# Performance work log

Measured on AMD Instinct MI355X. Metric: run time of the kernel, lower is better.

Reference implementation:

```python
import jax, jax.numpy as jnp
import numpy as np

H = 8
DH = 64  # attention_head_size
HID = 512
NEG = -90000000000.0

def _lin(x, w, b):
    return x @ w + b

def _tfs(x):  # [N, HID] -> [H, N, DH]
    n = x.shape[0]
    return x.reshape(n, H, DH).transpose(1, 0, 2)

def _cross(q, ck, v, cv, mask, dw, db):
    # q: [H,N,DH], ck/cv: [H,M,DH], v: [H,N,DH], mask: [N,M]
    s = jnp.einsum('hnd,hmd->hnm', q, ck)
    s = s * mask[None, :, :] / jnp.sqrt(jnp.asarray(DH, s.dtype))
    s = jnp.where(s == 0.0, NEG, s)  # faithful zero->-inf hack
    p = jax.nn.softmax(s, axis=-1)
    ctx = v + jnp.einsum('hnm,hmd->hnd', p, cv)  # residual add of raw value
    n = ctx.shape[1]
    ctx = ctx.transpose(1, 0, 2).reshape(n, H * DH)
    return _lin(ctx, dw, db)

def setup_inputs() -> dict:
    key = jax.random.key(0)
    ks = jax.random.split(key, 24)
    N1, N2, D1 = 4096, 4096, 300
    d = {}
    d['h_head'] = jax.random.normal(ks[0], (N1, D1), jnp.float32)
    d['h_tail'] = jax.random.normal(ks[1], (N2, HID), jnp.float32)
    d['batch_head'] = jnp.sort(jax.random.randint(ks[2], (N1,), 0, 64))
    d['batch_tail'] = jnp.sort(jax.random.randint(ks[3], (N2,), 0, 64))
    def w(k, i, o):
        return jax.random.normal(k, (i, o), jnp.float32) / np.sqrt(i)
    d['map_w'] = w(ks[4], D1, HID); d['map_b'] = jnp.zeros((HID,), jnp.float32)
    names = ['q1', 'k1', 'v1', 'q2', 'k2', 'v2', 'd1', 'd2']
    for i, nm in enumerate(names):
        d[nm + '_w'] = w(ks[5 + i], HID, HID)
        d[nm + '_b'] = jnp.zeros((HID,), jnp.float32)
    return d

def reference(h_head, h_tail, batch_head, batch_tail,
              map_w, map_b,
              q1_w, q1_b, k1_w, k1_b, v1_w, v1_b,
              q2_w, q2_b, k2_w, k2_b, v2_w, v2_b,
              d1_w, d1_b, d2_w, d2_b):
    hh = _lin(h_head, map_w, map_b)  # n_dim1 != n_dim2 -> map
    q_h = _tfs(_lin(hh, q1_w, q1_b))
    k_h = _tfs(_lin(hh, k1_w, k1_b))
    v_h = _tfs(_lin(hh, v1_w, v1_b))
    q_t = _tfs(_lin(h_tail, q2_w, q2_b))
    k_t = _tfs(_lin(h_tail, k2_w, k2_b))
    v_t = _tfs(_lin(h_tail, v2_w, v2_b))
    mask = (batch_head[:, None] == batch_tail[None, :]).astype(jnp.float32)
    out_head = _cross(q_h, k_t, v_h, v_t, mask, d1_w, d1_b)
    out_tail = _cross(q_t, k_h, v_t, v_h, mask.T, d2_w, d2_b)
    return (out_head, out_tail)
```

## Files before the change

kernel.cpp:

```cpp
#include <hip/hip_runtime.h>
#include <hip/hip_bf16.h>
#include <math.h>


typedef __bf16 bf16x8 __attribute__((ext_vector_type(8)));
typedef float  f32x4  __attribute__((ext_vector_type(4)));

#define HID 512
#define NTOK 4096

#define AS1(p) ((const __attribute__((address_space(1))) void*)(p))
#define AS3(p) ((__attribute__((address_space(3))) void*)(p))

struct PrepArgs {
    const float* h_head; const float* h_tail;
    const int* bh; const int* bt;
    const float* map_w; const float* map_b;
    const float* qkvw[3]; const float* qkvb[3];
    const float* tsrc[8]; __bf16* tdst[8];
    __bf16* hh_bf; __bf16* ht_bf; __bf16* mapw_bf;
    float* fb;
    int* ranges;
};

__global__ __launch_bounds__(256) void fused_prep(PrepArgs pa) {
    const int q = blockIdx.x, z = blockIdx.z, tid = threadIdx.x;
    __shared__ __bf16 T[64][72];

    if (z == 0) {
        if (q == 0 && tid < 128) {
            int b = tid & 63;
            const int* arr = (tid < 64) ? pa.bh : pa.bt;
            int base = (tid < 64) ? 0 : 128;
            int lo = 0, hi = NTOK;
            while (lo < hi) { int mid = (lo + hi) >> 1; if (arr[mid] < b) lo = mid + 1; else hi = mid; }
            int start = lo;
            lo = 0; hi = NTOK;
            while (lo < hi) { int mid = (lo + hi) >> 1; if (arr[mid] <= b) lo = mid + 1; else hi = mid; }
            pa.ranges[base + b] = start;
            pa.ranges[base + 64 + b] = lo;
        }
        for (int idx = tid; idx < 8 * 40; idx += 256) {
            int r   = q * 8 + idx / 40;
            int col = (idx % 40) * 8;
            bf16x8 v;
            if (col + 8 <= 300) {
                float4 f0 = *(const float4*)&pa.h_head[(size_t)r * 300 + col];
                float4 f1 = *(const float4*)&pa.h_head[(size_t)r * 300 + col + 4];
                v[0]=(__bf16)f0.x; v[1]=(__bf16)f0.y; v[2]=(__bf16)f0.z; v[3]=(__bf16)f0.w;
                v[4]=(__bf16)f1.x; v[5]=(__bf16)f1.y; v[6]=(__bf16)f1.z; v[7]=(__bf16)f1.w;
            } else if (col < 300) {
                float4 f0 = *(const float4*)&pa.h_head[(size_t)r * 300 + col];
                v[0]=(__bf16)f0.x; v[1]=(__bf16)f0.y; v[2]=(__bf16)f0.z; v[3]=(__bf16)f0.w;
                v[4]=(__bf16)0.f; v[5]=(__bf16)0.f; v[6]=(__bf16)0.f; v[7]=(__bf16)0.f;
            } else {
                #pragma unroll
                for (int j = 0; j < 8; ++j) v[j] = (__bf16)0.f;
            }
            *(bf16x8*)&pa.hh_bf[(size_t)r * 320 + col] = v;
        }
    } else if (z == 1) {
        for (int idx = tid; idx < 8 * 64; idx += 256) {
            int r   = q * 8 + (idx >> 6);
            int col = (idx & 63) * 8;
            float4 f0 = *(const float4*)&pa.h_tail[(size_t)r * 512 + col];
            float4 f1 = *(const float4*)&pa.h_tail[(size_t)r * 512 + col + 4];
            bf16x8 v;
            v[0]=(__bf16)f0.x; v[1]=(__bf16)f0.y; v[2]=(__bf16)f0.z; v[3]=(__bf16)f0.w;
            v[4]=(__bf16)f1.x; v[5]=(__bf16)f1.y; v[6]=(__bf16)f1.z; v[7]=(__bf16)f1.w;
            *(bf16x8*)&pa.ht_bf[(size_t)r * 512 + col] = v;
        }
    } else if (z == 2) {
        if (q < 96) {
            int r   = q * 4 + (tid >> 6);
            int col = (tid & 63) * 8;
            bf16x8 v;
            if (r < 300) {
                float4 f0 = *(const float4*)&pa.map_w[(size_t)r * 512 + col];
                float4 f1 = *(const float4*)&pa.map_w[(size_t)r * 512 + col + 4];
                v[0]=(__bf16)f0.x; v[1]=(__bf16)f0.y; v[2]=(__bf16)f0.z; v[3]=(__bf16)f0.w;
                v[4]=(__bf16)f1.x; v[5]=(__bf16)f1.y; v[6]=(__bf16)f1.z; v[7]=(__bf16)f1.w;
            } else {
                #pragma unroll
                for (int j = 0; j < 8; ++j) v[j] = (__bf16)0.f;
            }
            *(bf16x8*)&pa.mapw_bf[(size_t)r * 512 + col] = v;
        } else if (q < 102) {
            int b2 = q - 96;
            int w  = b2 >> 1;
            int n  = ((b2 & 1) << 8) + tid;
            const float* W = pa.qkvw[w];
            float s = pa.qkvb[w][n];
            for (int j = 0; j < 512; ++j)
                s += pa.map_b[j] * W[(size_t)j * 512 + n];
            pa.fb[w * 512 + n] = s;
        }
    } else {
        if (q >= 64) return;
        const int jz = z - 3;
        const float* src = pa.tsrc[jz];
        __bf16* dst = pa.tdst[jz];
        const int tk = (q >> 3) * 64;
        const int tn = (q & 7) * 64;
        const int r0 = tid >> 4;
        const int c0 = (tid & 15) * 4;
        #pragma unroll
        for (int i = 0; i < 4; ++i) {
            float4 v = *(const float4*)&src[(size_t)(tk + r0 + i * 16) * 512 + tn + c0];
            T[r0 + i * 16][c0 + 0] = (__bf16)v.x;
            T[r0 + i * 16][c0 + 1] = (__bf16)v.y;
            T[r0 + i * 16][c0 + 2] = (__bf16)v.z;
            T[r0 + i * 16][c0 + 3] = (__bf16)v.w;
        }
        __syncthreads();
        const int n  = tid >> 2;
        const int kk = (tid & 3) * 16;
        bf16x8 o0, o1;
        #pragma unroll
        for (int j = 0; j < 8; ++j) { o0[j] = T[kk + j][n]; o1[j] = T[kk + 8 + j][n]; }
        __bf16* dp = dst + (size_t)(tn + n) * 512 + tk + kk;
        *(bf16x8*)dp       = o0;
        *(bf16x8*)(dp + 8) = o1;
    }
}

struct GemmJobs {
    const __bf16* A[6];
    const __bf16* W[6];
    const float*  bias[6];
    void*         C[6];
    int           Kp[6];
    int           ldC[6];
    int           Ncol[6];
};

template <typename TC>
__global__ __launch_bounds__(256) void gemm128(GemmJobs jobs) {
    __shared__ __align__(16) __bf16 As[2][4096];
    __shared__ __align__(16) __bf16 Bs[2][4096];

    const int z = blockIdx.z;
    const __bf16* A    = jobs.A[z];
    const __bf16* W    = jobs.W[z];
    const float*  bias = jobs.bias[z];
    TC*           C    = (TC*)jobs.C[z];
    const int     Kp   = jobs.Kp[z];

    const int tid  = threadIdx.x;
    const int wave = tid >> 6;
    const int lane = tid & 63;
    const int quad = lane >> 4;
    const int l16  = lane & 15;
    const int wy   = wave >> 1;
    const int wx   = wave & 1;
    const int rowBase = blockIdx.y * 128;
    const int colBase = blockIdx.x * 128;

    const int s_row = tid >> 2;
    const int s_kc  = ((tid & 3) ^ ((s_row >> 1) & 3)) * 8;

    const __bf16* gA = A + (size_t)(rowBase + s_row) * Kp + s_kc;
    const __bf16* gB = W + (size_t)(colBase + s_row) * Kp + s_kc;
    const int waveOff = wave * 512;

    f32x4 acc[4][4] = {};
    const int nk = Kp >> 5;

    __builtin_amdgcn_global_load_lds(AS1(gA),                   AS3(&As[0][waveOff]),        16, 0, 0);
    __builtin_amdgcn_global_load_lds(AS1(gA + (size_t)64 * Kp), AS3(&As[0][2048 + waveOff]), 16, 0, 0);
    __builtin_amdgcn_global_load_lds(AS1(gB),                   AS3(&Bs[0][waveOff]),        16, 0, 0);
    __builtin_amdgcn_global_load_lds(AS1(gB + (size_t)64 * Kp), AS3(&Bs[0][2048 + waveOff]), 16, 0, 0);

    for (int i = 0; i < nk; ++i) {
        const int cur = i & 1;
        __syncthreads();

        if (i + 1 < nk) {
            const int kt = (i + 1) * 32;
            const int nx = cur ^ 1;
            __builtin_amdgcn_global_load_lds(AS1(gA + kt),                   AS3(&As[nx][waveOff]),        16, 0, 0);
            __builtin_amdgcn_global_load_lds(AS1(gA + kt + (size_t)64 * Kp), AS3(&As[nx][2048 + waveOff]), 16, 0, 0);
            __builtin_amdgcn_global_load_lds(AS1(gB + kt),                   AS3(&Bs[nx][waveOff]),        16, 0, 0);
            __builtin_amdgcn_global_load_lds(AS1(gB + kt + (size_t)64 * Kp), AS3(&Bs[nx][2048 + waveOff]), 16, 0, 0);
        }

        bf16x8 ar[4], br[4];
        #pragma unroll
        for (int ii = 0; ii < 4; ++ii) {
            const int ra = wy * 64 + ii * 16 + l16;
            ar[ii] = *(const bf16x8*)&As[cur][ra * 32 + ((quad ^ ((ra >> 1) & 3)) << 3)];
        }
        #pragma unroll
        for (int jj = 0; jj < 4; ++jj) {
            const int rb = wx * 64 + jj * 16 + l16;
            br[jj] = *(const bf16x8*)&Bs[cur][rb * 32 + ((quad ^ ((rb >> 1) & 3)) << 3)];
        }
        #pragma unroll
        for (int ii = 0; ii < 4; ++ii)
            #pragma unroll
            for (int jj = 0; jj < 4; ++jj)
                acc[ii][jj] = __builtin_amdgcn_mfma_f32_16x16x32_bf16(ar[ii], br[jj], acc[ii][jj], 0, 0, 0);
    }

    const int ldC  = jobs.ldC[z];
    const int Ncol = jobs.Ncol[z];
    #pragma unroll
    for (int jj = 0; jj < 4; ++jj) {
        int col = colBase + wx * 64 + jj * 16 + l16;
        if (col < Ncol) {
            float bv = bias ? bias[col] : 0.f;
            #pragma unroll
            for (int ii = 0; ii < 4; ++ii) {
                #pragma unroll
                for (int r = 0; r < 4; ++r) {
                    int row = rowBase + wy * 64 + ii * 16 + quad * 4 + r;
                    C[(size_t)row * ldC + col] = (TC)(acc[ii][jj][r] + bv);
                }
            }
        }
    }
}

__global__ __launch_bounds__(256) void attn_mfma(
    const __bf16* __restrict__ Q0, const __bf16* __restrict__ K0,
    const __bf16* __restrict__ Vr0, const __bf16* __restrict__ Vc0,
    const __bf16* __restrict__ Q1, const __bf16* __restrict__ K1,
    const __bf16* __restrict__ Vr1, const __bf16* __restrict__ Vc1,
    const int* __restrict__ ranges,
    __bf16* __restrict__ O0, __bf16* __restrict__ O1,
    int Nq, int Nk)
{
    __shared__ __align__(16) __bf16 Qs[64][72];
    __shared__ __align__(16) __bf16 Ks[64][72];
    __shared__ __align__(16) __bf16 Vt[64][72];
    __shared__ __align__(16) __bf16 Ps[64][72];

    const int z = blockIdx.z;
    const __bf16* Q    = z ? Q1 : Q0;
    const __bf16* Kg   = z ? K1 : K0;
    const __bf16* Vres = z ? Vr1 : Vr0;
    const __bf16* Vctx = z ? Vc1 : Vc0;
    __bf16* Out        = z ? O1 : O0;
    const int* qstart  = z ? ranges + 128 : ranges;
    const int* qend    = z ? ranges + 192 : ranges + 64;
    const int* kstart  = z ? ranges       : ranges + 128;
    const int* kend    = z ? ranges + 64  : ranges + 192;

    const int h = blockIdx.x, b = blockIdx.y;
    const int qs = qstart[b], qe = qend[b];
    const int ts = kstart[b], te = kend[b];
    const int nq = qe - qs, nk = te - ts;
    if (nq <= 0) return;

    const int tid  = threadIdx.x;
    const int wave = tid >> 6;
    const int lane = tid & 63;
    const int quad = lane >> 4;
    const int l16  = lane & 15;
    const int srow = tid >> 2;
    const int scol = (tid & 3) * 16;

    if (nk <= 0) {
        float* meanv = (float*)Qs;
        if (tid < 64) {
            float s = 0.f;
            for (int m = 0; m < Nk; ++m)
                s += (float)Vctx[(size_t)m * HID + h * 64 + tid];
            meanv[tid] = s / (float)Nk;
        }
        __syncthreads();
        int d = tid & 63;
        for (int r = qs + (tid >> 6); r < qe; r += 4) {
            size_t off = (size_t)r * HID + h * 64 + d;
            Out[off] = (__bf16)((float)Vres[off] + meanv[d]);
        }
        return;
    }

    for (int qc = 0; qc < nq; qc += 64) {
        __syncthreads();
        {
            int qg = min(qs + qc + srow, Nq - 1);
            const __bf16* src = Q + (size_t)qg * HID + h * 64 + scol;
            *(bf16x8*)&Qs[srow][scol]     = *(const bf16x8*)src;
            *(bf16x8*)&Qs[srow][scol + 8] = *(const bf16x8*)(src + 8);
        }
        __syncthreads();
        bf16x8 aq0 = *(const bf16x8*)&Qs[wave * 16 + l16][quad * 8];
        bf16x8 aq1 = *(const bf16x8*)&Qs[wave * 16 + l16][32 + quad * 8];

        f32x4 O[4] = {};
        float Mx[4], L[4];
        #pragma unroll
        for (int r = 0; r < 4; ++r) { Mx[r] = -__builtin_inff(); L[r] = 0.f; }

// ... 75 lines not shown
            #pragma unroll
            for (int c = 0; c < 4; ++c)
                #pragma unroll
                for (int r = 0; r < 4; ++r)
                    Ps[wave * 16 + quad * 4 + r][c * 16 + l16] = (__bf16)S[c][r];
            __syncthreads();

            bf16x8 ap0 = *(const bf16x8*)&Ps[wave * 16 + l16][quad * 8];
            bf16x8 ap1 = *(const bf16x8*)&Ps[wave * 16 + l16][32 + quad * 8];
            #pragma unroll
            for (int c = 0; c < 4; ++c) {
                bf16x8 bv0 = *(const bf16x8*)&Vt[c * 16 + l16][quad * 8];
                bf16x8 bv1 = *(const bf16x8*)&Vt[c * 16 + l16][32 + quad * 8];
                O[c] = __builtin_amdgcn_mfma_f32_16x16x32_bf16(ap0, bv0, O[c], 0, 0, 0);
                O[c] = __builtin_amdgcn_mfma_f32_16x16x32_bf16(ap1, bv1, O[c], 0, 0, 0);
            }
        }

        #pragma unroll
        for (int c = 0; c < 4; ++c) {
            int d = h * 64 + c * 16 + l16;
            #pragma unroll
            for (int r = 0; r < 4; ++r) {
                int qrow = qs + qc + wave * 16 + quad * 4 + r;
                if (qrow < qe) {
                    size_t off = (size_t)qrow * HID + d;
                    Out[off] = (__bf16)((float)Vres[off] + O[c][r] / L[r]);
                }
            }
        }
    }
}

extern "C" void kernel_launch(void* const* d_in, const int* in_sizes, int n_in,
                              void* d_out, int out_size, void* d_ws, size_t ws_size,
                              hipStream_t stream) {
    (void)in_sizes; (void)n_in; (void)out_size; (void)ws_size;

    const float* h_head = (const float*)d_in[0];
    const float* h_tail = (const float*)d_in[1];
    const int* batch_head = (const int*)d_in[2];
    const int* batch_tail = (const int*)d_in[3];
    const float* map_w = (const float*)d_in[4];
    const float* map_b = (const float*)d_in[5];
    const float* q1_w = (const float*)d_in[6];
    const float* q1_b = (const float*)d_in[7];
    const float* k1_w = (const float*)d_in[8];
    const float* k1_b = (const float*)d_in[9];
    const float* v1_w = (const float*)d_in[10];
    const float* v1_b = (const float*)d_in[11];
    const float* q2_w = (const float*)d_in[12];
    const float* q2_b = (const float*)d_in[13];
    const float* k2_w = (const float*)d_in[14];
    const float* k2_b = (const float*)d_in[15];
    const float* v2_w = (const float*)d_in[16];
    const float* v2_b = (const float*)d_in[17];
    const float* d1_w = (const float*)d_in[18];
    const float* d1_b = (const float*)d_in[19];
    const float* d2_w = (const float*)d_in[20];
    const float* d2_b = (const float*)d_in[21];

    float* out = (float*)d_out;

    const size_t SZ = (size_t)NTOK * HID;
    char* ws = (char*)d_ws;
    int* ranges   = (int*)ws;
    __bf16* hh_bf = (__bf16*)(ws + 1024);
    __bf16* ht_bf = hh_bf + (size_t)NTOK * 320;
    __bf16* mapw_bf = ht_bf + SZ;
    __bf16* q1T  = mapw_bf + 384 * 512;
    __bf16* k1T  = q1T + 512 * 512;
    __bf16* v1T  = k1T + 512 * 512;
    __bf16* q2T  = v1T + 512 * 512;
    __bf16* k2T  = q2T + 512 * 512;
    __bf16* v2T  = k2T + 512 * 512;
    __bf16* d1T  = v2T + 512 * 512;
    __bf16* d2T  = d1T + 512 * 512;
    __bf16* FqT  = d2T + 512 * 512;
    __bf16* FkT  = FqT + 512 * 320;
    __bf16* FvT  = FkT + 512 * 320;
    __bf16* qh   = FvT + 512 * 320;
    __bf16* kh   = qh  + SZ;
    __bf16* vh   = kh  + SZ;
    __bf16* qt   = vh  + SZ;
    __bf16* kt   = qt  + SZ;
    __bf16* vt   = kt  + SZ;
    __bf16* ctxh = vt  + SZ;
    __bf16* ctxt = ctxh + SZ;
    float*  fb   = (float*)(ctxt + SZ);

    PrepArgs pa;
    pa.h_head = h_head; pa.h_tail = h_tail;
    pa.bh = batch_head; pa.bt = batch_tail;
    pa.map_w = map_w; pa.map_b = map_b;
    pa.qkvw[0] = q1_w; pa.qkvw[1] = k1_w; pa.qkvw[2] = v1_w;
    pa.qkvb[0] = q1_b; pa.qkvb[1] = k1_b; pa.qkvb[2] = v1_b;
    const float* wsrc[8] = {q1_w, k1_w, v1_w, q2_w, k2_w, v2_w, d1_w, d2_w};
    __bf16* wdst[8] = {q1T, k1T, v1T, q2T, k2T, v2T, d1T, d2T};
    for (int i = 0; i < 8; ++i) { pa.tsrc[i] = wsrc[i]; pa.tdst[i] = wdst[i]; }
    pa.hh_bf = hh_bf; pa.ht_bf = ht_bf; pa.mapw_bf = mapw_bf;
    pa.fb = fb; pa.ranges = ranges;
    fused_prep<<<dim3(512, 1, 11), dim3(256), 0, stream>>>(pa);

    {
        GemmJobs j;
        const __bf16* a3[3] = {q1T, k1T, v1T};
        __bf16* c3[3] = {FqT, FkT, FvT};
        for (int i = 0; i < 6; ++i) {
            int s = i < 3 ? i : 0;
            j.A[i] = a3[s]; j.W[i] = mapw_bf; j.bias[i] = nullptr;
            j.C[i] = c3[s]; j.Kp[i] = 512; j.ldC[i] = 320; j.Ncol[i] = 320;
        }
        gemm128<__bf16><<<dim3(3, 4, 3), dim3(256), 0, stream>>>(j);
    }

    {
        GemmJobs j;
        j.A[0] = hh_bf; j.W[0] = FqT; j.bias[0] = fb;        j.C[0] = qh; j.Kp[0] = 320;
        j.A[1] = hh_bf; j.W[1] = FkT; j.bias[1] = fb + 512;  j.C[1] = kh; j.Kp[1] = 320;
        j.A[2] = hh_bf; j.W[2] = FvT; j.bias[2] = fb + 1024; j.C[2] = vh; j.Kp[2] = 320;
        j.A[3] = ht_bf; j.W[3] = q2T; j.bias[3] = q2_b;      j.C[3] = qt; j.Kp[3] = 512;
        j.A[4] = ht_bf; j.W[4] = k2T; j.bias[4] = k2_b;      j.C[4] = kt; j.Kp[4] = 512;
        j.A[5] = ht_bf; j.W[5] = v2T; j.bias[5] = v2_b;      j.C[5] = vt; j.Kp[5] = 512;
        for (int i = 0; i < 6; ++i) { j.ldC[i] = HID; j.Ncol[i] = HID; }
        gemm128<__bf16><<<dim3(4, 32, 6), dim3(256), 0, stream>>>(j);
    }

    attn_mfma<<<dim3(8, 64, 2), dim3(256), 0, stream>>>(
        qh, kt, vh, vt,
        qt, kh, vt, vh,
        ranges, ctxh, ctxt, NTOK, NTOK);

    {
        GemmJobs j;
        for (int i = 0; i < 6; ++i) {
            int s = i < 2 ? i : 0;
            j.A[i] = s ? ctxt : ctxh;
            j.W[i] = s ? d2T : d1T;
            j.bias[i] = s ? d2_b : d1_b;
            j.C[i] = s ? (void*)(out + SZ) : (void*)out;
            j.Kp[i] = 512; j.ldC[i] = HID; j.Ncol[i] = HID;
        }
        gemm128<float><<<dim3(4, 32, 2), dim3(256), 0, stream>>>(j);
    }
}
```

Before: 193.8 us.

## Fuse all stages into a persistent megakernel with software grid barriers

Replaces the five separate kernel launches (prep, F-gemm, QKV gemm, attention, output gemm) with one persistent kernel that loops over virtual blocks per stage and separates stages with atomic-counter grid barriers. The map_b bias reduction is also split across four waves with a shared-memory reduction. The aim is to remove launch gaps and tail idle time between stages. In exchange it adds barrier spin overhead and a memset, limits the grid to the co-resident block count, and constrains occupancy to the shared 36 KB LDS footprint.

Result: slower. 393.6 us (+103.1%).

```diff
diff --git a/kernel.cpp b/kernel.cpp
--- a/kernel.cpp
+++ b/kernel.cpp
@@ -12,139 +12,49 @@
 #define AS1(p) ((const __attribute__((address_space(1))) void*)(p))
 #define AS3(p) ((__attribute__((address_space(3))) void*)(p))
 
-struct PrepArgs {
+struct MegaArgs {
     const float* h_head; const float* h_tail;
     const int* bh; const int* bt;
     const float* map_w; const float* map_b;
-    const float* qkvw[3]; const float* qkvb[3];
-    const float* tsrc[8]; __bf16* tdst[8];
-    __bf16* hh_bf; __bf16* ht_bf; __bf16* mapw_bf;
+    const float* wsrc[8];
+    const float* qkvb1[3];
+    const float* b2[3];
+    const float* d1_b; const float* d2_b;
+    __bf16* wT[8];
+    __bf16* hh_bf;
+    __bf16* ht_bf;
+    __bf16* mapw_bf;
+    __bf16* F[3];
+    __bf16* qh; __bf16* kh; __bf16* vh;
+    __bf16* qt; __bf16* kt; __bf16* vt;
+    __bf16* ctxh; __bf16* ctxt;
     float* fb;
     int* ranges;
+    float* out;
+    int* bar;
+    int nblk;
 };
 
-__global__ __launch_bounds__(256) void fused_prep(PrepArgs pa) {
-    const int q = blockIdx.x, z = blockIdx.z, tid = threadIdx.x;
-    __shared__ __bf16 T[64][72];
-
-    if (z == 0) {
-        if (q == 0 && tid < 128) {
-            int b = tid & 63;
-            const int* arr = (tid < 64) ? pa.bh : pa.bt;
-            int base = (tid < 64) ? 0 : 128;
-            int lo = 0, hi = NTOK;
-            while (lo < hi) { int mid = (lo + hi) >> 1; if (arr[mid] < b) lo = mid + 1; else hi = mid; }
-            int start = lo;
-            lo = 0; hi = NTOK;
-            while (lo < hi) { int mid = (lo + hi) >> 1; if (arr[mid] <= b) lo = mid + 1; else hi = mid; }
-            pa.ranges[base + b] = start;
-            pa.ranges[base + 64 + b] = lo;
-        }
-        for (int idx = tid; idx < 8 * 40; idx += 256) {
-            int r   = q * 8 + idx / 40;
-            int col = (idx % 40) * 8;
-            bf16x8 v;
-            if (col + 8 <= 300) {
-                float4 f0 = *(const float4*)&pa.h_head[(size_t)r * 300 + col];
-                float4 f1 = *(const float4*)&pa.h_head[(size_t)r * 300 + col + 4];
-                v[0]=(__bf16)f0.x; v[1]=(__bf16)f0.y; v[2]=(__bf16)f0.z; v[3]=(__bf16)f0.w;
-                v[4]=(__bf16)f1.x; v[5]=(__bf16)f1.y; v[6]=(__bf16)f1.z; v[7]=(__bf16)f1.w;
-            } else if (col < 300) {
-                float4 f0 = *(const float4*)&pa.h_head[(size_t)r * 300 + col];
-                v[0]=(__bf16)f0.x; v[1]=(__bf16)f0.y; v[2]=(__bf16)f0.z; v[3]=(__bf16)f0.w;
-                v[4]=(__bf16)0.f; v[5]=(__bf16)0.f; v[6]=(__bf16)0.f; v[7]=(__bf16)0.f;
-            } else {
-                #pragma unroll
-                for (int j = 0; j < 8; ++j) v[j] = (__bf16)0.f;
-            }
-            *(bf16x8*)&pa.hh_bf[(size_t)r * 320 + col] = v;
-        }
-    } else if (z == 1) {
-        for (int idx = tid; idx < 8 * 64; idx += 256) {
-            int r   = q * 8 + (idx >> 6);
-            int col = (idx & 63) * 8;
-            float4 f0 = *(const float4*)&pa.h_tail[(size_t)r * 512 + col];
-            float4 f1 = *(const float4*)&pa.h_tail[(size_t)r * 512 + col + 4];
-            bf16x8 v;
-            v[0]=(__bf16)f0.x; v[1]=(__bf16)f0.y; v[2]=(__bf16)f0.z; v[3]=(__bf16)f0.w;
-            v[4]=(__bf16)f1.x; v[5]=(__bf16)f1.y; v[6]=(__bf16)f1.z; v[7]=(__bf16)f1.w;
-            *(bf16x8*)&pa.ht_bf[(size_t)r * 512 + col] = v;
-        }
-    } else if (z == 2) {
-        if (q < 96) {
-            int r   = q * 4 + (tid >> 6);
-            int col = (tid & 63) * 8;
-            bf16x8 v;
-            if (r < 300) {
-                float4 f0 = *(const float4*)&pa.map_w[(size_t)r * 512 + col];
-                float4 f1 = *(const float4*)&pa.map_w[(size_t)r * 512 + col + 4];
-                v[0]=(__bf16)f0.x; v[1]=(__bf16)f0.y; v[2]=(__bf16)f0.z; v[3]=(__bf16)f0.w;
-                v[4]=(__bf16)f1.x; v[5]=(__bf16)f1.y; v[6]=(__bf16)f1.z; v[7]=(__bf16)f1.w;
-            } else {
-                #pragma unroll
-                for (int j = 0; j < 8; ++j) v[j] = (__bf16)0.f;
-            }
-            *(bf16x8*)&pa.mapw_bf[(size_t)r * 512 + col] = v;
-        } else if (q < 102) {
-            int b2 = q - 96;
-            int w  = b2 >> 1;
-            int n  = ((b2 & 1) << 8) + tid;
-            const float* W = pa.qkvw[w];
-            float s = pa.qkvb[w][n];
-            for (int j = 0; j < 512; ++j)
-                s += pa.map_b[j] * W[(size_t)j * 512 + n];
-            pa.fb[w * 512 + n] = s;
-        }
-    } else {
-        if (q >= 64) return;
-        const int jz = z - 3;
-        const float* src = pa.tsrc[jz];
-        __bf16* dst = pa.tdst[jz];
-        const int tk = (q >> 3) * 64;
-        const int tn = (q & 7) * 64;
-        const int r0 = tid >> 4;
-        const int c0 = (tid & 15) * 4;
-        #pragma unroll
-        for (int i = 0; i < 4; ++i) {
-            float4 v = *(const float4*)&src[(size_t)(tk + r0 + i * 16) * 512 + tn + c0];
-            T[r0 + i * 16][c0 + 0] = (__bf16)v.x;
-            T[r0 + i * 16][c0 + 1] = (__bf16)v.y;
-            T[r0 + i * 16][c0 + 2] = (__bf16)v.z;
-            T[r0 + i * 16][c0 + 3] = (__bf16)v.w;
-        }
-        __syncthreads();
-        const int n  = tid >> 2;
-        const int kk = (tid & 3) * 16;
-        bf16x8 o0, o1;
-        #pragma unroll
-        for (int j = 0; j < 8; ++j) { o0[j] = T[kk + j][n]; o1[j] = T[kk + 8 + j][n]; }
-        __bf16* dp = dst + (size_t)(tn + n) * 512 + tk + kk;
-        *(bf16x8*)dp       = o0;
-        *(bf16x8*)(dp + 8) = o1;
-    }
+__device__ __forceinline__ void grid_barrier(int* cnt, int nblk) {
+    __syncthreads();
+    __threadfence();
+    if (threadIdx.x == 0) {
+        __hip_atomic_fetch_add(cnt, 1, __ATOMIC_RELAXED, __HIP_MEMORY_SCOPE_AGENT);
+        while (__hip_atomic_load(cnt, __ATOMIC_RELAXED, __HIP_MEMORY_SCOPE_AGENT) < nblk)
+            __builtin_amdgcn_s_sleep(8);
+    }
+    __syncthreads();
+    __threadfence();
 }
 
-struct GemmJobs {
-    const __bf16* A[6];
-    const __bf16* W[6];
-    const float*  bias[6];
-    void*         C[6];
-    int           Kp[6];
-    int           ldC[6];
-    int           Ncol[6];
-};
-
 template <typename TC>
-__global__ __launch_bounds__(256) void gemm128(GemmJobs jobs) {
-    __shared__ __align__(16) __bf16 As[2][4096];
-    __shared__ __align__(16) __bf16 Bs[2][4096];
-
-    const int z = blockIdx.z;
-    const __bf16* A    = jobs.A[z];
-    const __bf16* W    = jobs.W[z];
-    const float*  bias = jobs.bias[z];
-    TC*           C    = (TC*)jobs.C[z];
-    const int     Kp   = jobs.Kp[z];
+__device__ __forceinline__ void gemm_tile(
+    const __bf16* __restrict__ A, const __bf16* __restrict__ W,
+    const float* __restrict__ bias, TC* __restrict__ C,
+    int Kp, int ldC, int Ncol, int bx, int by, char* SMEM)
+{
+    __bf16* As = (__bf16*)SMEM;
+    __bf16* Bs = (__bf16*)(SMEM + 16384);
 
     const int tid  = threadIdx.x;
     const int wave = tid >> 6;
@@ -153,8 +63,8 @@
     const int l16  = lane & 15;
     const int wy   = wave >> 1;
     const int wx   = wave & 1;
-    const int rowBase = blockIdx.y * 128;
-    const int colBase = blockIdx.x * 128;
+    const int rowBase = by * 128;
+    const int colBase = bx * 128;
 
     const int s_row = tid >> 2;
     const int s_kc  = ((tid & 3) ^ ((s_row >> 1) & 3)) * 8;
@@ -166,10 +76,12 @@
     f32x4 acc[4][4] = {};
     const int nk = Kp >> 5;
 
-    __builtin_amdgcn_global_load_lds(AS1(gA),                   AS3(&As[0][waveOff]),        16, 0, 0);
-    __builtin_amdgcn_global_load_lds(AS1(gA + (size_t)64 * Kp), AS3(&As[0][2048 + waveOff]), 16, 0, 0);
-    __builtin_amdgcn_global_load_lds(AS1(gB),                   AS3(&Bs[0][waveOff]),        16, 0, 0);
-    __builtin_amdgcn_global_load_lds(AS1(gB + (size_t)64 * Kp), AS3(&Bs[0][2048 + waveOff]), 16, 0, 0);
+    __syncthreads();
+
+    __builtin_amdgcn_global_load_lds(AS1(gA),                   AS3(&As[waveOff]),        16, 0, 0);
+    __builtin_amdgcn_global_load_lds(AS1(gA + (size_t)64 * Kp), AS3(&As[2048 + waveOff]), 16, 0, 0);
+    __builtin_amdgcn_global_load_lds(AS1(gB),                   AS3(&Bs[waveOff]),        16, 0, 0);
+    __builtin_amdgcn_global_load_lds(AS1(gB + (size_t)64 * Kp), AS3(&Bs[2048 + waveOff]), 16, 0, 0);
 
     for (int i = 0; i < nk; ++i) {
         const int cur = i & 1;
@@ -178,22 +90,22 @@
         if (i + 1 < nk) {
             const int kt = (i + 1) * 32;
             const int nx = cur ^ 1;
-            __builtin_amdgcn_global_load_lds(AS1(gA + kt),                   AS3(&As[nx][waveOff]),        16, 0, 0);
-            __builtin_amdgcn_global_load_lds(AS1(gA + kt + (size_t)64 * Kp), AS3(&As[nx][2048 + waveOff]), 16, 0, 0);
-            __builtin_amdgcn_global_load_lds(AS1(gB + kt),                   AS3(&Bs[nx][waveOff]),        16, 0, 0);
-            __builtin_amdgcn_global_load_lds(AS1(gB + kt + (size_t)64 * Kp), AS3(&Bs[nx][2048 + waveOff]), 16, 0, 0);
+            __builtin_amdgcn_global_load_lds(AS1(gA + kt),                   AS3(&As[nx * 4096 + waveOff]),        16, 0, 0);
+            __builtin_amdgcn_global_load_lds(AS1(gA + kt + (size_t)64 * Kp), AS3(&As[nx * 4096 + 2048 + waveOff]), 16, 0, 0);
+            __builtin_amdgcn_global_load_lds(AS1(gB + kt),                   AS3(&Bs[nx * 4096 + waveOff]),        16, 0, 0);
+            __builtin_amdgcn_global_load_lds(AS1(gB + kt + (size_t)64 * Kp), AS3(&Bs[nx * 4096 + 2048 + waveOff]), 16, 0, 0);
         }
 
         bf16x8 ar[4], br[4];
         #pragma unroll
         for (int ii = 0; ii < 4; ++ii) {
             const int ra = wy * 64 + ii * 16 + l16;
-            ar[ii] = *(const bf16x8*)&As[cur][ra * 32 + ((quad ^ ((ra >> 1) & 3)) << 3)];
+            ar[ii] = *(const bf16x8*)&As[cur * 4096 + ra * 32 + ((quad ^ ((ra >> 1) & 3)) << 3)];
         }
         #pragma unroll
         for (int jj = 0; jj < 4; ++jj) {
             const int rb = wx * 64 + jj * 16 + l16;
-            br[jj] = *(const bf16x8*)&Bs[cur][rb * 32 + ((quad ^ ((rb >> 1) & 3)) << 3)];
+            br[jj] = *(const bf16x8*)&Bs[cur * 4096 + rb * 32 + ((quad ^ ((rb >> 1) & 3)) << 3)];
         }
         #pragma unroll
         for (int ii = 0; ii < 4; ++ii)
@@ -202,8 +114,6 @@
                 acc[ii][jj] = __builtin_amdgcn_mfma_f32_16x16x32_bf16(ar[ii], br[jj], acc[ii][jj], 0, 0, 0);
     }
 
-    const int ldC  = jobs.ldC[z];
-    const int Ncol = jobs.Ncol[z];
     #pragma unroll
     for (int jj = 0; jj < 4; ++jj) {
         int col = colBase + wx * 64 + jj * 16 + l16;
@@ -221,32 +131,26 @@
     }
 }
 
-__global__ __launch_bounds__(256) void attn_mfma(
-    const __bf16* __restrict__ Q0, const __bf16* __restrict__ K0,
-    const __bf16* __restrict__ Vr0, const __bf16* __restrict__ Vc0,
-    const __bf16* __restrict__ Q1, const __bf16* __restrict__ K1,
-    const __bf16* __restrict__ Vr1, const __bf16* __restrict__ Vc1,
-    const int* __restrict__ ranges,
-    __bf16* __restrict__ O0, __bf16* __restrict__ O1,
-    int Nq, int Nk)
+__device__ void attn_block(const MegaArgs& a, int h, int b, int z, char* SMEM)
 {
-    __shared__ __align__(16) __bf16 Qs[64][72];
-    __shared__ __align__(16) __bf16 Ks[64][72];
-    __shared__ __align__(16) __bf16 Vt[64][72];
-    __shared__ __align__(16) __bf16 Ps[64][72];
-
-    const int z = blockIdx.z;
-    const __bf16* Q    = z ? Q1 : Q0;
-    const __bf16* Kg   = z ? K1 : K0;
-    const __bf16* Vres = z ? Vr1 : Vr0;
-    const __bf16* Vctx = z ? Vc1 : Vc0;
-    __bf16* Out        = z ? O1 : O0;
+    typedef __bf16 row72[72];
+    row72* Qs = (row72*)SMEM;
+    row72* Ks = (row72*)(SMEM + 9216);
+    row72* Vt = (row72*)(SMEM + 18432);
+    row72* Ps = (row72*)(SMEM + 27648);
+
+    const __bf16* Q    = z ? a.qt : a.qh;
+    const __bf16* Kg   = z ? a.kh : a.kt;
+    const __bf16* Vres = z ? a.vt : a.vh;
+    const __bf16* Vctx = z ? a.vh : a.vt;
+    __bf16* Out        = z ? a.ctxt : a.ctxh;
+    const int* ranges  = a.ranges;
     const int* qstart  = z ? ranges + 128 : ranges;
     const int* qend    = z ? ranges + 192 : ranges + 64;
     const int* kstart  = z ? ranges       : ranges + 128;
     const int* kend    = z ? ranges + 64  : ranges + 192;
-
-    const int h = blockIdx.x, b = blockIdx.y;
+    const int Nq = NTOK, Nk = NTOK;
+
     const int qs = qstart[b], qe = qend[b];
     const int ts = kstart[b], te = kend[b];
     const int nq = qe - qs, nk = te - ts;
@@ -261,6 +165,7 @@
     const int scol = (tid & 3) * 16;
 
     if (nk <= 0) {
+        __syncthreads();
         float* meanv = (float*)Qs;
         if (tid < 64) {
             float s = 0.f;
@@ -402,115 +307,231 @@
     }
 }
 
+__global__ __launch_bounds__(256, 2) void mega(MegaArgs a) {
+    __shared__ __align__(16) char SMEM[36864];
+    const int nblk = a.nblk;
+    const int tid = threadIdx.x;
+
+    for (int vb = blockIdx.x; vb < 1656; vb += nblk) {
+        if (vb < 512) {
+            const int q = vb;
+            if (q == 0 && tid < 128) {
+                int b = tid & 63;
+                const int* arr = (tid < 64) ? a.bh : a.bt;
+                int base = (tid < 64) ? 0 : 128;
+                int lo = 0, hi = NTOK;
+                while (lo < hi) { int mid = (lo + hi) >> 1; if (arr[mid] < b) lo = mid + 1; else hi = mid; }
+                int start = lo;
+                lo = 0; hi = NTOK;
+                while (lo < hi) { int mid = (lo + hi) >> 1; if (arr[mid] <= b) lo = mid + 1; else hi = mid; }
+                a.ranges[base + b] = start;
+                a.ranges[base + 64 + b] = lo;
+            }
+            for (int idx = tid; idx < 8 * 40; idx += 256) {
+                int r   = q * 8 + idx / 40;
+                int col = (idx % 40) * 8;
+                bf16x8 v;
+                if (col + 8 <= 300) {
+                    float4 f0 = *(const float4*)&a.h_head[(size_t)r * 300 + col];
+                    float4 f1 = *(const float4*)&a.h_head[(size_t)r * 300 + col + 4];
+                    v[0]=(__bf16)f0.x; v[1]=(__bf16)f0.y; v[2]=(__bf16)f0.z; v[3]=(__bf16)f0.w;
+                    v[4]=(__bf16)f1.x; v[5]=(__bf16)f1.y; v[6]=(__bf16)f1.z; v[7]=(__bf16)f1.w;
+                } else if (col < 300) {
+                    float4 f0 = *(const float4*)&a.h_head[(size_t)r * 300 + col];
+                    v[0]=(__bf16)f0.x; v[1]=(__bf16)f0.y; v[2]=(__bf16)f0.z; v[3]=(__bf16)f0.w;
+                    v[4]=(__bf16)0.f; v[5]=(__bf16)0.f; v[6]=(__bf16)0.f; v[7]=(__bf16)0.f;
+                } else {
+                    #pragma unroll
+                    for (int j = 0; j < 8; ++j) v[j] = (__bf16)0.f;
+                }
+                *(bf16x8*)&a.hh_bf[(size_t)r * 320 + col] = v;
+            }
+        } else if (vb < 1024) {
+            const int q = vb - 512;
+            for (int idx = tid; idx < 8 * 64; idx += 256) {
+                int r   = q * 8 + (idx >> 6);
+                int col = (idx & 63) * 8;
+                float4 f0 = *(const float4*)&a.h_tail[(size_t)r * 512 + col];
+                float4 f1 = *(const float4*)&a.h_tail[(size_t)r * 512 + col + 4];
+                bf16x8 v;
+                v[0]=(__bf16)f0.x; v[1]=(__bf16)f0.y; v[2]=(__bf16)f0.z; v[3]=(__bf16)f0.w;
+                v[4]=(__bf16)f1.x; v[5]=(__bf16)f1.y; v[6]=(__bf16)f1.z; v[7]=(__bf16)f1.w;
+                *(bf16x8*)&a.ht_bf[(size_t)r * 512 + col] = v;
+            }
+        } else if (vb < 1120) {
+            const int q = vb - 1024;
+            int r   = q * 4 + (tid >> 6);
+            int col = (tid & 63) * 8;
+            bf16x8 v;
+            if (r < 300) {
+                float4 f0 = *(const float4*)&a.map_w[(size_t)r * 512 + col];
+                float4 f1 = *(const float4*)&a.map_w[(size_t)r * 512 + col + 4];
+                v[0]=(__bf16)f0.x; v[1]=(__bf16)f0.y; v[2]=(__bf16)f0.z; v[3]=(__bf16)f0.w;
+                v[4]=(__bf16)f1.x; v[5]=(__bf16)f1.y; v[6]=(__bf16)f1.z; v[7]=(__bf16)f1.w;
+            } else {
+                #pragma unroll
+                for (int j = 0; j < 8; ++j) v[j] = (__bf16)0.f;
+            }
+            *(bf16x8*)&a.mapw_bf[(size_t)r * 512 + col] = v;
+        } else if (vb < 1144) {
+            __syncthreads();
+            float* red = (float*)SMEM;
+            const int i  = vb - 1120;
+            const int w  = i >> 3;
+            const int c8 = i & 7;
+            const int n  = c8 * 64 + (tid & 63);
+            const int jq = tid >> 6;
+            const float* W = a.wsrc[w];
+            float s = 0.f;
+            for (int j = jq * 128; j < jq * 128 + 128; ++j)
+                s += a.map_b[j] * W[(size_t)j * 512 + n];
+            red[tid] = s;
+            __syncthreads();
+            if (tid < 64) {
+                float r4 = red[tid] + red[64 + tid] + red[128 + tid] + red[192 + tid]
+                         + a.qkvb1[w][c8 * 64 + tid];
+                a.fb[w * 512 + c8 * 64 + tid] = r4;
+            }
+        } else {
+            __syncthreads();
+            typedef __bf16 trow[72];
+            trow* T = (trow*)SMEM;
+            const int i  = vb - 1144;
+            const int jz = i >> 6;
+            const int q  = i & 63;
+            const float* src = a.wsrc[jz];
+            __bf16* dst = a.wT[jz];
+            const int tk = (q >> 3) * 64;
+            const int tn = (q & 7) * 64;
+            const int r0 = tid >> 4;
+            const int c0 = (tid & 15) * 4;
+            #pragma unroll
+            for (int ii = 0; ii < 4; ++ii) {
+                float4 v = *(const float4*)&src[(size_t)(tk + r0 + ii * 16) * 512 + tn + c0];
+                T[r0 + ii * 16][c0 + 0] = (__bf16)v.x;
+                T[r0 + ii * 16][c0 + 1] = (__bf16)v.y;
+                T[r0 + ii * 16][c0 + 2] = (__bf16)v.z;
+                T[r0 + ii * 16][c0 + 3] = (__bf16)v.w;
+            }
+            __syncthreads();
+            const int n  = tid >> 2;
+            const int kk = (tid & 3) * 16;
+            bf16x8 o0, o1;
+            #pragma unroll
+            for (int j = 0; j < 8; ++j) { o0[j] = T[kk + j][n]; o1[j] = T[kk + 8 + j][n]; }
+            __bf16* dp = dst + (size_t)(tn + n) * 512 + tk + kk;
+            *(bf16x8*)dp       = o0;
+            *(bf16x8*)(dp + 8) = o1;
+        }
+    }
+    grid_barrier(a.bar + 0, nblk);
+
+    for (int vb = blockIdx.x; vb < 36; vb += nblk) {
+        const int z  = vb % 3;
+        const int t  = vb / 3;
+        const int bx = t % 3;
+        const int by = t / 3;
+        gemm_tile<__bf16>(a.wT[z], a.mapw_bf, nullptr, a.F[z], 512, 320, 320, bx, by, SMEM);
+    }
+    grid_barrier(a.bar + 16, nblk);
+
+    for (int vb = blockIdx.x; vb < 768; vb += nblk) {
+        const int z  = vb >> 7;
+        const int r  = vb & 127;
+        const int bx = r & 3;
+        const int by = r >> 2;
+        const __bf16* Aj; const __bf16* Wj; const float* bj; __bf16* Cj; int Kpj;
+        if (z < 3) {
+            Aj = a.hh_bf; Wj = a.F[z]; bj = a.fb + z * 512;
+            Cj = (z == 0) ? a.qh : (z == 1) ? a.kh : a.vh;
+            Kpj = 320;
+        } else {
+            Aj = a.ht_bf; Wj = a.wT[z]; bj = a.b2[z - 3];
+            Cj = (z == 3) ? a.qt : (z == 4) ? a.kt : a.vt;
+            Kpj = 512;
+        }
+        gemm_tile<__bf16>(Aj, Wj, bj, Cj, Kpj, HID, HID, bx, by, SMEM);
+    }
+    grid_barrier(a.bar + 32, nblk);
+
+    for (int vb = blockIdx.x; vb < 1024; vb += nblk) {
+        const int h = vb & 7;
+        const int b = (vb >> 3) & 63;
+        const int z = vb >> 9;
+        attn_block(a, h, b, z, SMEM);
+    }
+    grid_barrier(a.bar + 48, nblk);
+
+    for (int vb = blockIdx.x; vb < 256; vb += nblk) {
+        const int z  = vb >> 7;
+        const int r  = vb & 127;
+        const int bx = r & 3;
+        const int by = r >> 2;
+        const __bf16* Aj = z ? a.ctxt : a.ctxh;
+        const __bf16* Wj = z ? a.wT[7] : a.wT[6];
+        const float*  bj = z ? a.d2_b : a.d1_b;
+        float* Cj = a.out + (size_t)z * NTOK * HID;
+        gemm_tile<float>(Aj, Wj, bj, Cj, 512, HID, HID, bx, by, SMEM);
+    }
+}
+
 extern "C" void kernel_launch(void* const* d_in, const int* in_sizes, int n_in,
                               void* d_out, int out_size, void* d_ws, size_t ws_size,
                               hipStream_t stream) {
     (void)in_sizes; (void)n_in; (void)out_size; (void)ws_size;
 
-    const float* h_head = (const float*)d_in[0];
-    const float* h_tail = (const float*)d_in[1];
-    const int* batch_head = (const int*)d_in[2];
-    const int* batch_tail = (const int*)d_in[3];
-    const float* map_w = (const float*)d_in[4];
-    const float* map_b = (const float*)d_in[5];
-    const float* q1_w = (const float*)d_in[6];
-    const float* q1_b = (const float*)d_in[7];
-    const float* k1_w = (const float*)d_in[8];
-    const float* k1_b = (const float*)d_in[9];
-    const float* v1_w = (const float*)d_in[10];
-    const float* v1_b = (const float*)d_in[11];
-    const float* q2_w = (const float*)d_in[12];
-    const float* q2_b = (const float*)d_in[13];
-    const float* k2_w = (const float*)d_in[14];
-    const float* k2_b = (const float*)d_in[15];
-    const float* v2_w = (const float*)d_in[16];
-    const float* v2_b = (const float*)d_in[17];
-    const float* d1_w = (const float*)d_in[18];
-    const float* d1_b = (const float*)d_in[19];
-    const float* d2_w = (const float*)d_in[20];
-    const float* d2_b = (const float*)d_in[21];
-
-    float* out = (float*)d_out;
-
     const size_t SZ = (size_t)NTOK * HID;
     char* ws = (char*)d_ws;
-    int* ranges   = (int*)ws;
-    __bf16* hh_bf = (__bf16*)(ws + 1024);
+    int* bar      = (int*)ws;
+    int* ranges   = (int*)(ws + 512);
+    __bf16* hh_bf = (__bf16*)(ws + 2048);
     __bf16* ht_bf = hh_bf + (size_t)NTOK * 320;
-    __bf16* mapw_bf = ht_bf + SZ;
-    __bf16* q1T  = mapw_bf + 384 * 512;
-    __bf16* k1T  = q1T + 512 * 512;
-    __bf16* v1T  = k1T + 512 * 512;
-    __bf16* q2T  = v1T + 512 * 512;
-    __bf16* k2T  = q2T + 512 * 512;
-    __bf16* v2T  = k2T + 512 * 512;
-    __bf16* d1T  = v2T + 512 * 512;
-    __bf16* d2T  = d1T + 512 * 512;
-    __bf16* FqT  = d2T + 512 * 512;
-    __bf16* FkT  = FqT + 512 * 320;
-    __bf16* FvT  = FkT + 512 * 320;
-    __bf16* qh   = FvT + 512 * 320;
-    __bf16* kh   = qh  + SZ;
-    __bf16* vh   = kh  + SZ;
-    __bf16* qt   = vh  + SZ;
-    __bf16* kt   = qt  + SZ;
-    __bf16* vt   = kt  + SZ;
-    __bf16* ctxh = vt  + SZ;
-    __bf16* ctxt = ctxh + SZ;
-    float*  fb   = (float*)(ctxt + SZ);
-
-    PrepArgs pa;
-    pa.h_head = h_head; pa.h_tail = h_tail;
-    pa.bh = batch_head; pa.bt = batch_tail;
-    pa.map_w = map_w; pa.map_b = map_b;
-    pa.qkvw[0] = q1_w; pa.qkvw[1] = k1_w; pa.qkvw[2] = v1_w;
-    pa.qkvb[0] = q1_b; pa.qkvb[1] = k1_b; pa.qkvb[2] = v1_b;
-    const float* wsrc[8] = {q1_w, k1_w, v1_w, q2_w, k2_w, v2_w, d1_w, d2_w};
-    __bf16* wdst[8] = {q1T, k1T, v1T, q2T, k2T, v2T, d1T, d2T};
-    for (int i = 0; i < 8; ++i) { pa.tsrc[i] = wsrc[i]; pa.tdst[i] = wdst[i]; }
-    pa.hh_bf = hh_bf; pa.ht_bf = ht_bf; pa.mapw_bf = mapw_bf;
-    pa.fb = fb; pa.ranges = ranges;
-    fused_prep<<<dim3(512, 1, 11), dim3(256), 0, stream>>>(pa);
-
-    {
-        GemmJobs j;
-        const __bf16* a3[3] = {q1T, k1T, v1T};
-        __bf16* c3[3] = {FqT, FkT, FvT};
-        for (int i = 0; i < 6; ++i) {
-            int s = i < 3 ? i : 0;
-            j.A[i] = a3[s]; j.W[i] = mapw_bf; j.bias[i] = nullptr;
-            j.C[i] = c3[s]; j.Kp[i] = 512; j.ldC[i] = 320; j.Ncol[i] = 320;
-        }
-        gemm128<__bf16><<<dim3(3, 4, 3), dim3(256), 0, stream>>>(j);
-    }
-
-    {
-        GemmJobs j;
-        j.A[0] = hh_bf; j.W[0] = FqT; j.bias[0] = fb;        j.C[0] = qh; j.Kp[0] = 320;
-        j.A[1] = hh_bf; j.W[1] = FkT; j.bias[1] = fb + 512;  j.C[1] = kh; j.Kp[1] = 320;
-        j.A[2] = hh_bf; j.W[2] = FvT; j.bias[2] = fb + 1024; j.C[2] = vh; j.Kp[2] = 320;
-        j.A[3] = ht_bf; j.W[3] = q2T; j.bias[3] = q2_b;      j.C[3] = qt; j.Kp[3] = 512;
-        j.A[4] = ht_bf; j.W[4] = k2T; j.bias[4] = k2_b;      j.C[4] = kt; j.Kp[4] = 512;
-        j.A[5] = ht_bf; j.W[5] = v2T; j.bias[5] = v2_b;      j.C[5] = vt; j.Kp[5] = 512;
-        for (int i = 0; i < 6; ++i) { j.ldC[i] = HID; j.Ncol[i] = HID; }
-        gemm128<__bf16><<<dim3(4, 32, 6), dim3(256), 0, stream>>>(j);
-    }
-
-    attn_mfma<<<dim3(8, 64, 2), dim3(256), 0, stream>>>(
-        qh, kt, vh, vt,
-        qt, kh, vt, vh,
-        ranges, ctxh, ctxt, NTOK, NTOK);
-
-    {
-        GemmJobs j;
-        for (int i = 0; i < 6; ++i) {
-            int s = i < 2 ? i : 0;
-            j.A[i] = s ? ctxt : ctxh;
-            j.W[i] = s ? d2T : d1T;
-            j.bias[i] = s ? d2_b : d1_b;
-            j.C[i] = s ? (void*)(out + SZ) : (void*)out;
-            j.Kp[i] = 512; j.ldC[i] = HID; j.Ncol[i] = HID;
-        }
-        gemm128<float><<<dim3(4, 32, 2), dim3(256), 0, stream>>>(j);
-    }
+    __bf16* mapw  = ht_bf + SZ;
+    __bf16* wT0   = mapw + 384 * 512;
+    __bf16* F0    = wT0 + 8 * 512 * 512;
+    __bf16* qh    = F0 + 3 * 512 * 320;
+    float*  fb    = (float*)(qh + 8 * SZ);
+
+    MegaArgs a;
+    a.h_head = (const float*)d_in[0];
+    a.h_tail = (const float*)d_in[1];
+    a.bh     = (const int*)d_in[2];
+    a.bt     = (const int*)d_in[3];
+    a.map_w  = (const float*)d_in[4];
+    a.map_b  = (const float*)d_in[5];
+    for (int i = 0; i < 8; ++i) a.wsrc[i] = (const float*)d_in[6 + 2 * i];
+    a.qkvb1[0] = (const float*)d_in[7];
+    a.qkvb1[1] = (const float*)d_in[9];
+    a.qkvb1[2] = (const float*)d_in[11];
+    a.b2[0]    = (const float*)d_in[13];
+    a.b2[1]    = (const float*)d_in[15];
+    a.b2[2]    = (const float*)d_in[17];
+    a.d1_b     = (const float*)d_in[19];
+    a.d2_b     = (const float*)d_in[21];
+
+    for (int i = 0; i < 8; ++i) a.wT[i] = wT0 + (size_t)i * 512 * 512;
+    a.hh_bf = hh_bf; a.ht_bf = ht_bf; a.mapw_bf = mapw;
+    for (int i = 0; i < 3; ++i) a.F[i] = F0 + (size_t)i * 512 * 320;
+    a.qh = qh;            a.kh = qh + SZ;       a.vh = qh + 2 * SZ;
+    a.qt = qh + 3 * SZ;   a.kt = qh + 4 * SZ;   a.vt = qh + 5 * SZ;
+    a.ctxh = qh + 6 * SZ; a.ctxt = qh + 7 * SZ;
+    a.fb = fb; a.ranges = ranges;
+    a.out = (float*)d_out;
+    a.bar = bar;
+
+    static int g_nblk = 0;
+    if (g_nblk == 0) {
+        int dev = 0, ncu = 0, occ = 0;
+        hipGetDevice(&dev);
+        hipDeviceGetAttribute(&ncu, hipDeviceAttributeMultiprocessorCount, dev);
+        hipOccupancyMaxActiveBlocksPerMultiprocessor(&occ, mega, 256, 0);
+        if (ncu < 1) ncu = 256;
+        if (occ < 1) occ = 1;
+        long cap = (long)occ * (long)ncu;
+        g_nblk = (int)(cap < 768 ? cap : 768);
+    }
+    a.nblk = g_nblk;
+
+    hipMemsetAsync(bar, 0, 256, stream);
+    mega<<<dim3(g_nblk), dim3(256), 0, stream>>>(a);
 }
```

## Merge tail QKV projections into weight-fold GEMM launch and split bias-fold reduction

Applied to the files above, without the earlier changes.

The tail-side Q/K/V projections (independent of the map weight fold) now run in the same launch as the small FqT/FkT/FvT fold GEMMs, via a shared device gemm body dispatched by block index. This fills the otherwise tiny 36-block launch with 384 more blocks. The following head-side GEMM launch shrinks to 3 jobs. The bias-fold dot products in the prep kernel are also spread over more blocks, with a 4-way shared-memory reduction instead of one thread looping over 512 elements, which shortens the serial tail of the prep kernel.

New measurement: 200.6 us. 3.5% more time.

```diff
diff --git a/kernel.cpp b/kernel.cpp
--- a/kernel.cpp
+++ b/kernel.cpp
@@ -25,7 +25,7 @@
 
 __global__ __launch_bounds__(256) void fused_prep(PrepArgs pa) {
     const int q = blockIdx.x, z = blockIdx.z, tid = threadIdx.x;
-    __shared__ __bf16 T[64][72];
+    __shared__ __align__(16) __bf16 T[64][72];
 
     if (z == 0) {
         if (q == 0 && tid < 128) {
@@ -85,15 +85,24 @@
                 for (int j = 0; j < 8; ++j) v[j] = (__bf16)0.f;
             }
             *(bf16x8*)&pa.mapw_bf[(size_t)r * 512 + col] = v;
-        } else if (q < 102) {
-            int b2 = q - 96;
-            int w  = b2 >> 1;
-            int n  = ((b2 & 1) << 8) + tid;
+        } else if (q < 120) {
+            float* red = (float*)T;
+            const int i  = q - 96;
+            const int w  = i >> 3;
+            const int c8 = i & 7;
+            const int n  = c8 * 64 + (tid & 63);
+            const int jq = tid >> 6;
             const float* W = pa.qkvw[w];
-            float s = pa.qkvb[w][n];
-            for (int j = 0; j < 512; ++j)
+            float s = 0.f;
+            for (int j = jq * 128; j < jq * 128 + 128; ++j)
                 s += pa.map_b[j] * W[(size_t)j * 512 + n];
-            pa.fb[w * 512 + n] = s;
+            red[tid] = s;
+            __syncthreads();
+            if (tid < 64) {
+                float r4 = red[tid] + red[64 + tid] + red[128 + tid] + red[192 + tid]
+                         + pa.qkvb[w][c8 * 64 + tid];
+                pa.fb[w * 512 + c8 * 64 + tid] = r4;
+            }
         }
     } else {
         if (q >= 64) return;
@@ -124,28 +133,13 @@
     }
 }
 
-struct GemmJobs {
-    const __bf16* A[6];
-    const __bf16* W[6];
-    const float*  bias[6];
-    void*         C[6];
-    int           Kp[6];
-    int           ldC[6];
-    int           Ncol[6];
-};
-
 template <typename TC>
-__global__ __launch_bounds__(256) void gemm128(GemmJobs jobs) {
-    __shared__ __align__(16) __bf16 As[2][4096];
-    __shared__ __align__(16) __bf16 Bs[2][4096];
-
-    const int z = blockIdx.z;
-    const __bf16* A    = jobs.A[z];
-    const __bf16* W    = jobs.W[z];
-    const float*  bias = jobs.bias[z];
-    TC*           C    = (TC*)jobs.C[z];
-    const int     Kp   = jobs.Kp[z];
-
+__device__ __forceinline__ void gemm_body(
+    const __bf16* __restrict__ A, const __bf16* __restrict__ W,
+    const float* __restrict__ bias, TC* __restrict__ C,
+    int Kp, int ldC, int Ncol, int bx, int by,
+    __bf16* As, __bf16* Bs)
+{
     const int tid  = threadIdx.x;
     const int wave = tid >> 6;
     const int lane = tid & 63;
@@ -153,8 +147,8 @@
     const int l16  = lane & 15;
     const int wy   = wave >> 1;
     const int wx   = wave & 1;
-    const int rowBase = blockIdx.y * 128;
-    const int colBase = blockIdx.x * 128;
+    const int rowBase = by * 128;
+    const int colBase = bx * 128;
 
     const int s_row = tid >> 2;
     const int s_kc  = ((tid & 3) ^ ((s_row >> 1) & 3)) * 8;
@@ -166,10 +160,10 @@
     f32x4 acc[4][4] = {};
     const int nk = Kp >> 5;
 
-    __builtin_amdgcn_global_load_lds(AS1(gA),                   AS3(&As[0][waveOff]),        16, 0, 0);
-    __builtin_amdgcn_global_load_lds(AS1(gA + (size_t)64 * Kp), AS3(&As[0][2048 + waveOff]), 16, 0, 0);
-    __builtin_amdgcn_global_load_lds(AS1(gB),                   AS3(&Bs[0][waveOff]),        16, 0, 0);
-    __builtin_amdgcn_global_load_lds(AS1(gB + (size_t)64 * Kp), AS3(&Bs[0][2048 + waveOff]), 16, 0, 0);
+    __builtin_amdgcn_global_load_lds(AS1(gA),                   AS3(&As[waveOff]),        16, 0, 0);
+    __builtin_amdgcn_global_load_lds(AS1(gA + (size_t)64 * Kp), AS3(&As[2048 + waveOff]), 16, 0, 0);
+    __builtin_amdgcn_global_load_lds(AS1(gB),                   AS3(&Bs[waveOff]),        16, 0, 0);
+    __builtin_amdgcn_global_load_lds(AS1(gB + (size_t)64 * Kp), AS3(&Bs[2048 + waveOff]), 16, 0, 0);
 
     for (int i = 0; i < nk; ++i) {
         const int cur = i & 1;
@@ -178,22 +172,22 @@
         if (i + 1 < nk) {
             const int kt = (i + 1) * 32;
             const int nx = cur ^ 1;
-            __builtin_amdgcn_global_load_lds(AS1(gA + kt),                   AS3(&As[nx][waveOff]),        16, 0, 0);
-            __builtin_amdgcn_global_load_lds(AS1(gA + kt + (size_t)64 * Kp), AS3(&As[nx][2048 + waveOff]), 16, 0, 0);
-            __builtin_amdgcn_global_load_lds(AS1(gB + kt),                   AS3(&Bs[nx][waveOff]),        16, 0, 0);
-            __builtin_amdgcn_global_load_lds(AS1(gB + kt + (size_t)64 * Kp), AS3(&Bs[nx][2048 + waveOff]), 16, 0, 0);
+            __builtin_amdgcn_global_load_lds(AS1(gA + kt),                   AS3(&As[nx * 4096 + waveOff]),        16, 0, 0);
+            __builtin_amdgcn_global_load_lds(AS1(gA + kt + (size_t)64 * Kp), AS3(&As[nx * 4096 + 2048 + waveOff]), 16, 0, 0);
+            __builtin_amdgcn_global_load_lds(AS1(gB + kt),                   AS3(&Bs[nx * 4096 + waveOff]),        16, 0, 0);
+            __builtin_amdgcn_global_load_lds(AS1(gB + kt + (size_t)64 * Kp), AS3(&Bs[nx * 4096 + 2048 + waveOff]), 16, 0, 0);
         }
 
         bf16x8 ar[4], br[4];
         #pragma unroll
         for (int ii = 0; ii < 4; ++ii) {
             const int ra = wy * 64 + ii * 16 + l16;
-            ar[ii] = *(const bf16x8*)&As[cur][ra * 32 + ((quad ^ ((ra >> 1) & 3)) << 3)];
+            ar[ii] = *(const bf16x8*)&As[cur * 4096 + ra * 32 + ((quad ^ ((ra >> 1) & 3)) << 3)];
         }
         #pragma unroll
         for (int jj = 0; jj < 4; ++jj) {
             const int rb = wx * 64 + jj * 16 + l16;
-            br[jj] = *(const bf16x8*)&Bs[cur][rb * 32 + ((quad ^ ((rb >> 1) & 3)) << 3)];
+            br[jj] = *(const bf16x8*)&Bs[cur * 4096 + rb * 32 + ((quad ^ ((rb >> 1) & 3)) << 3)];
         }
         #pragma unroll
         for (int ii = 0; ii < 4; ++ii)
@@ -202,8 +196,6 @@
                 acc[ii][jj] = __builtin_amdgcn_mfma_f32_16x16x32_bf16(ar[ii], br[jj], acc[ii][jj], 0, 0, 0);
     }
 
-    const int ldC  = jobs.ldC[z];
-    const int Ncol = jobs.Ncol[z];
     #pragma unroll
     for (int jj = 0; jj < 4; ++jj) {
         int col = colBase + wx * 64 + jj * 16 + l16;
@@ -218,6 +210,50 @@
                 }
             }
         }
+    }
+}
+
+struct GemmJobs {
+    const __bf16* A[3];
+    const __bf16* W[3];
+    const float*  bias[3];
+    void*         C[3];
+    int           Kp[3];
+};
+
+template <typename TC>
+__global__ __launch_bounds__(256) void gemm128(GemmJobs jobs) {
+    __shared__ __align__(16) __bf16 As[2][4096];
+    __shared__ __align__(16) __bf16 Bs[2][4096];
+    const int z = blockIdx.z;
+    gemm_body<TC>(jobs.A[z], jobs.W[z], jobs.bias[z], (TC*)jobs.C[z],
+                  jobs.Kp[z], HID, HID, blockIdx.x, blockIdx.y,
+                  &As[0][0], &Bs[0][0]);
+}
+
+struct D2Args {
+    const __bf16* wT1[3];
+    const __bf16* mapw;
+    __bf16*       F[3];
+    const __bf16* ht;
+    const __bf16* w2T[3];
+    const float*  b2[3];
+    __bf16*       out2[3];
+};
+
+__global__ __launch_bounds__(256) void gemm_d2(D2Args d) {
+    __shared__ __align__(16) __bf16 As[2][4096];
+    __shared__ __align__(16) __bf16 Bs[2][4096];
+    const int vb = blockIdx.x;
+    if (vb < 36) {
+        const int f = vb / 12, t = vb % 12;
+        gemm_body<__bf16>(d.wT1[f], d.mapw, nullptr, d.F[f],
+                          512, 320, 320, t % 3, t / 3, &As[0][0], &Bs[0][0]);
+    } else {
+        const int u = vb - 36;
+        const int w = u >> 7, t = u & 127;
+        gemm_body<__bf16>(d.ht, d.w2T[w], d.b2[w], d.out2[w],
+                          512, HID, HID, t & 3, t >> 2, &As[0][0], &Bs[0][0]);
     }
 }
 
@@ -473,15 +509,15 @@
     fused_prep<<<dim3(512, 1, 11), dim3(256), 0, stream>>>(pa);
 
     {
-        GemmJobs j;
-        const __bf16* a3[3] = {q1T, k1T, v1T};
-        __bf16* c3[3] = {FqT, FkT, FvT};
-        for (int i = 0; i < 6; ++i) {
-            int s = i < 3 ? i : 0;
-            j.A[i] = a3[s]; j.W[i] = mapw_bf; j.bias[i] = nullptr;
-            j.C[i] = c3[s]; j.Kp[i] = 512; j.ldC[i] = 320; j.Ncol[i] = 320;
-        }
-        gemm128<__bf16><<<dim3(3, 4, 3), dim3(256), 0, stream>>>(j);
+        D2Args d;
+        d.wT1[0] = q1T; d.wT1[1] = k1T; d.wT1[2] = v1T;
+        d.mapw = mapw_bf;
+        d.F[0] = FqT; d.F[1] = FkT; d.F[2] = FvT;
+        d.ht = ht_bf;
+        d.w2T[0] = q2T; d.w2T[1] = k2T; d.w2T[2] = v2T;
+        d.b2[0] = q2_b; d.b2[1] = k2_b; d.b2[2] = v2_b;
+        d.out2[0] = qt; d.out2[1] = kt; d.out2[2] = vt;
+        gemm_d2<<<dim3(420, 1, 1), dim3(256), 0, stream>>>(d);
     }
 
     {
@@ -489,11 +525,7 @@
         j.A[0] = hh_bf; j.W[0] = FqT; j.bias[0] = fb;        j.C[0] = qh; j.Kp[0] = 320;
         j.A[1] = hh_bf; j.W[1] = FkT; j.bias[1] = fb + 512;  j.C[1] = kh; j.Kp[1] = 320;
         j.A[2] = hh_bf; j.W[2] = FvT; j.bias[2] = fb + 1024; j.C[2] = vh; j.Kp[2] = 320;
-        j.A[3] = ht_bf; j.W[3] = q2T; j.bias[3] = q2_b;      j.C[3] = qt; j.Kp[3] = 512;
-        j.A[4] = ht_bf; j.W[4] = k2T; j.bias[4] = k2_b;      j.C[4] = kt; j.Kp[4] = 512;
-        j.A[5] = ht_bf; j.W[5] = v2T; j.bias[5] = v2_b;      j.C[5] = vt; j.Kp[5] = 512;
-        for (int i = 0; i < 6; ++i) { j.ldC[i] = HID; j.Ncol[i] = HID; }
-        gemm128<__bf16><<<dim3(4, 32, 6), dim3(256), 0, stream>>>(j);
+        gemm128<__bf16><<<dim3(4, 32, 3), dim3(256), 0, stream>>>(j);
     }
 
     attn_mfma<<<dim3(8, 64, 2), dim3(256), 0, stream>>>(
@@ -503,14 +535,9 @@
 
     {
         GemmJobs j;
-        for (int i = 0; i < 6; ++i) {
-            int s = i < 2 ? i : 0;
-            j.A[i] = s ? ctxt : ctxh;
-            j.W[i] = s ? d2T : d1T;
-            j.bias[i] = s ? d2_b : d1_b;
-            j.C[i] = s ? (void*)(out + SZ) : (void*)out;
-            j.Kp[i] = 512; j.ldC[i] = HID; j.Ncol[i] = HID;
-        }
+        j.A[0] = ctxh; j.W[0] = d1T; j.bias[0] = d1_b; j.C[0] = out;      j.Kp[0] = 512;
+        j.A[1] = ctxt; j.W[1] = d2T; j.bias[1] = d2_b; j.C[1] = out + SZ; j.Kp[1] = 512;
+        j.A[2] = ctxt; j.W[2] = d2T; j.bias[2] = d2_b; j.C[2] = out + SZ; j.Kp[2] = 512;
         gemm128<float><<<dim3(4, 32, 2), dim3(256), 0, stream>>>(j);
     }
 }
```
